# Optimization experiments

Measured on AMD Instinct MI355X. Metric: run time of the kernel, lower is better.

The kernel has to match this reference:

```python
import jax, jax.numpy as jnp
import numpy as np

N = 100000   # nodes
E = 1600000  # edges (avg degree 16)
N_IN, N_HID, N_OUT = 64, 64, 16


def setup_inputs() -> dict:
    key = jax.random.key(0)
    k1, k2, k3, k4 = jax.random.split(key, 4)
    x = jax.random.normal(k1, (N, N_IN), dtype=jnp.float32)
    edge_index = jax.random.randint(k2, (2, E), 0, N, dtype=jnp.int64)
    # Glorot-style init like PyG GCNConv linear weights
    W1 = jax.random.normal(k3, (N_IN, N_HID), dtype=jnp.float32) * (1.0 / np.sqrt(N_IN))
    b1 = jnp.zeros((N_HID,), dtype=jnp.float32)
    W2 = jax.random.normal(k4, (N_HID, N_OUT), dtype=jnp.float32) * (1.0 / np.sqrt(N_HID))
    b2 = jnp.zeros((N_OUT,), dtype=jnp.float32)
    return {"x": x, "edge_index": edge_index, "W1": W1, "b1": b1, "W2": W2, "b2": b2}


def reference(x, edge_index, W1, b1, W2, b2):
    n = x.shape[0]
    # GCNConv default: add self-loops with weight 1, symmetric normalization
    loop = jnp.arange(n, dtype=edge_index.dtype)
    src = jnp.concatenate([edge_index[0], loop])  # [E+N]
    dst = jnp.concatenate([edge_index[1], loop])  # [E+N]
    w = jnp.ones(src.shape[0], dtype=x.dtype)
    deg = jax.ops.segment_sum(w, dst, num_segments=n)           # in-degree incl. self-loop
    dinv = jnp.where(deg > 0, jax.lax.rsqrt(deg), 0.0)
    norm = dinv[src] * w * dinv[dst]                            # [E+N] edge coefficients

    def gcn_conv(h, Wm, bm):
        h = h @ Wm                                              # [N, d_out] linear first (PyG order)
        msg = h[src] * norm[:, None]                            # gather + scale
        return jax.ops.segment_sum(msg, dst, num_segments=n) + bm  # scatter-add + bias

    h = jax.nn.relu(gcn_conv(x, W1, b1))
    # dropout is identity at inference (training=False)
    return jax.nn.log_softmax(gcn_conv(h, W2, b2), axis=1)
```

## Files before the change

### kernel.cpp

```cpp
#include <hip/hip_runtime.h>

constexpr int FIN = 64;
constexpr int FH  = 64;
constexpr int FO  = 16;


constexpr int BSH      = 7;
constexpr int BW       = 1 << BSH;
constexpr int NBUCK    = 1024;
constexpr int EPB      = 4096;

constexpr int XSTR     = 68;

__device__ inline unsigned short f2bf(float f) {
    unsigned u = __float_as_uint(f);
    return (unsigned short)((u + 0x7FFFu + ((u >> 16) & 1u)) >> 16);
}
__device__ inline float bf2f(unsigned short h) {
    return __uint_as_float((unsigned)h << 16);
}
__device__ inline float4 bf4_to_f4(ushort4 u) {
    float4 f;
    f.x = bf2f(u.x); f.y = bf2f(u.y); f.z = bf2f(u.z); f.w = bf2f(u.w);
    return f;
}

__launch_bounds__(256)
__global__ void hist_kernel(const int* __restrict__ ei, int E,
                            unsigned short* __restrict__ gchist) {
    __shared__ int lh[NBUCK];
    int t = threadIdx.x;
    for (int i = t; i < NBUCK; i += 256) lh[i] = 0;
    __syncthreads();
    int base = blockIdx.x * EPB;
    int lim  = min(E, base + EPB);
    for (int e0 = base + t; e0 < lim; e0 += 2048) {
        int dd[8];
        #pragma unroll
        for (int q = 0; q < 8; ++q) {
            int e = e0 + q * 256;
            dd[q] = (e < lim) ? ei[E + e] : -1;
        }
        #pragma unroll
        for (int q = 0; q < 8; ++q)
            if (dd[q] >= 0) atomicAdd(&lh[dd[q] >> BSH], 1);
    }
    __syncthreads();
    unsigned short* gh = gchist + (size_t)blockIdx.x * NBUCK;
    for (int b = t; b < NBUCK; b += 256)
        gh[b] = (unsigned short)lh[b];
}

__launch_bounds__(1024)
__global__ void bucket_scan_kernel(const unsigned short* __restrict__ gchist,
                                   int* __restrict__ bbase, int* __restrict__ gbase,
                                   int NCH, int* __restrict__ offs, int N, int E) {
    __shared__ int s[NBUCK];
    int t = threadIdx.x;
    int v = 0;
    #pragma unroll 8
    for (int c = 0; c < NCH; ++c)
        v += (int)gchist[(size_t)c * NBUCK + t];
    s[t] = v;
    __syncthreads();
    for (int d = 1; d < NBUCK; d <<= 1) {
        int u = (t >= d) ? s[t - d] : 0;
        __syncthreads();
        s[t] += u;
        __syncthreads();
    }
    int ex = s[t] - v;
    bbase[t] = ex;
    if (t == NBUCK - 1) {
        bbase[NBUCK] = s[t];
        offs[N] = E;
    }
    int run = ex;
    #pragma unroll 8
    for (int c = 0; c < NCH; ++c) {
        gbase[(size_t)c * NBUCK + t] = run;
        run += (int)gchist[(size_t)c * NBUCK + t];
    }
}

__device__ inline void binning_body(const int* __restrict__ ei, int E, int chunk,
                                    const int* __restrict__ gbase,
                                    unsigned* __restrict__ ebuf, int* lh) {
    int t = threadIdx.x;
    const int* gb = gbase + (size_t)chunk * NBUCK;
    for (int i = t; i < NBUCK; i += 256) lh[i] = gb[i];
    __syncthreads();
    int base = chunk * EPB;
    int lim  = min(E, base + EPB);
    for (int e0 = base + t; e0 < lim; e0 += 2048) {
        int dd[8], ss[8];
        #pragma unroll
        for (int q = 0; q < 8; ++q) {
            int e = e0 + q * 256;
            if (e < lim) { dd[q] = ei[E + e]; ss[q] = ei[e]; } else dd[q] = -1;
        }
        #pragma unroll
        for (int q = 0; q < 8; ++q) {
            if (dd[q] >= 0) {
                int pos = atomicAdd(&lh[dd[q] >> BSH], 1);
                ebuf[pos] = (unsigned)ss[q] | ((unsigned)(dd[q] & (BW - 1)) << 17);
            }
        }
    }
}

__launch_bounds__(256)
__global__ void binning_kernel(const int* __restrict__ ei, int E,
                               const int* __restrict__ gbase, unsigned* __restrict__ ebuf) {
    __shared__ int lh[NBUCK];
    binning_body(ei, E, blockIdx.x, gbase, ebuf, lh);
}

__launch_bounds__(256, 4)
__global__ void gemm1_binning_kernel(const float* __restrict__ x, const float* __restrict__ W1,
                                     unsigned short* __restrict__ hsb,
                                     const int* __restrict__ ei, int E,
                                     const int* __restrict__ gbase, unsigned* __restrict__ ebuf,
                                     int N, int NBIN) {
    __shared__ float smem[FIN * FH + 64 * XSTR];
    int tid = threadIdx.x;
    if ((int)blockIdx.x < NBIN) {
        binning_body(ei, E, (int)blockIdx.x, gbase, ebuf, (int*)smem);
        return;
    }
    float* Ws = smem;
    float* Xs = smem + FIN * FH;
    int rowBase = ((int)blockIdx.x - NBIN) * 64;
    {
        const float4* W14 = (const float4*)W1;
        float4* Ws4 = (float4*)Ws;
        #pragma unroll
        for (int i = tid; i < 1024; i += 256) Ws4[i] = W14[i];
        const float4* x4 = (const float4*)x;
        #pragma unroll
        for (int i = tid; i < 1024; i += 256) {
            int row = i >> 4, kq = i & 15;
            int gr = min(rowBase + row, N - 1);
            *(float4*)&Xs[row * XSTR + kq * 4] = x4[(size_t)gr * 16 + kq];
        }
    }
    __syncthreads();
    int cg = tid & 15;
    int rg = tid >> 4;
    int r0 = rowBase + rg * 4;
    float4 acc0 = {0,0,0,0}, acc1 = {0,0,0,0}, acc2 = {0,0,0,0}, acc3 = {0,0,0,0};
    #pragma unroll 2
    for (int kc = 0; kc < 16; ++kc) {
        float4 xa0 = *(const float4*)&Xs[(rg * 4 + 0) * XSTR + kc * 4];
        float4 xa1 = *(const float4*)&Xs[(rg * 4 + 1) * XSTR + kc * 4];
        float4 xa2 = *(const float4*)&Xs[(rg * 4 + 2) * XSTR + kc * 4];
        float4 xa3 = *(const float4*)&Xs[(rg * 4 + 3) * XSTR + kc * 4];
        const float* xa0f = (const float*)&xa0;
        const float* xa1f = (const float*)&xa1;
        const float* xa2f = (const float*)&xa2;
        const float* xa3f = (const float*)&xa3;
        #pragma unroll
        for (int j = 0; j < 4; ++j) {
            float4 wv = *(const float4*)&Ws[(kc * 4 + j) * FH + cg * 4];
            float v0 = xa0f[j], v1 = xa1f[j], v2 = xa2f[j], v3 = xa3f[j];
            acc0.x = fmaf(v0, wv.x, acc0.x); acc0.y = fmaf(v0, wv.y, acc0.y);
            acc0.z = fmaf(v0, wv.z, acc0.z); acc0.w = fmaf(v0, wv.w, acc0.w);
            acc1.x = fmaf(v1, wv.x, acc1.x); acc1.y = fmaf(v1, wv.y, acc1.y);
            acc1.z = fmaf(v1, wv.z, acc1.z); acc1.w = fmaf(v1, wv.w, acc1.w);
            acc2.x = fmaf(v2, wv.x, acc2.x); acc2.y = fmaf(v2, wv.y, acc2.y);
            acc2.z = fmaf(v2, wv.z, acc2.z); acc2.w = fmaf(v2, wv.w, acc2.w);
            acc3.x = fmaf(v3, wv.x, acc3.x); acc3.y = fmaf(v3, wv.y, acc3.y);
            acc3.z = fmaf(v3, wv.z, acc3.z); acc3.w = fmaf(v3, wv.w, acc3.w);
        }
    }
    ushort4* hsb4 = (ushort4*)hsb;
    if (r0 + 0 < N) hsb4[(size_t)(r0 + 0) * 16 + cg] =
        make_ushort4(f2bf(acc0.x), f2bf(acc0.y), f2bf(acc0.z), f2bf(acc0.w));
    if (r0 + 1 < N) hsb4[(size_t)(r0 + 1) * 16 + cg] =
        make_ushort4(f2bf(acc1.x), f2bf(acc1.y), f2bf(acc1.z), f2bf(acc1.w));
    if (r0 + 2 < N) hsb4[(size_t)(r0 + 2) * 16 + cg] =
        make_ushort4(f2bf(acc2.x), f2bf(acc2.y), f2bf(acc2.z), f2bf(acc2.w));
    if (r0 + 3 < N) hsb4[(size_t)(r0 + 3) * 16 + cg] =
        make_ushort4(f2bf(acc3.x), f2bf(acc3.y), f2bf(acc3.z), f2bf(acc3.w));
}

__launch_bounds__(256)
__global__ void bucket_csr_kernel(const unsigned* __restrict__ ebuf,
                                  const int* __restrict__ bbase,
                                  int* __restrict__ csr, int* __restrict__ offs,
                                  float* __restrict__ dinv, int N) {
    __shared__ int cnt[BW], sc[BW], cur[BW];
    int t = threadIdx.x;
    int b = blockIdx.x;
    if (t < BW) cnt[t] = 0;
    __syncthreads();
    int beg = bbase[b], end = bbase[b + 1];
    for (int i0 = beg + t; i0 < end; i0 += 2048) {
        unsigned ww[8];
        #pragma unroll
        for (int q = 0; q < 8; ++q) {
            int i = i0 + q * 256;
            ww[q] = (i < end) ? ebuf[i] : 0xFFFFFFFFu;
        }
        #pragma unroll
        for (int q = 0; q < 8; ++q)
            if (ww[q] != 0xFFFFFFFFu) atomicAdd(&cnt[ww[q] >> 17], 1);
    }
    __syncthreads();
    if (t < BW) sc[t] = cnt[t];
    __syncthreads();
    for (int d = 1; d < BW; d <<= 1) {
        int u = (t < BW && t >= d) ? sc[t - d] : 0;
        __syncthreads();
        if (t < BW) sc[t] += u;
        __syncthreads();
    }
    int nodeBase = b << BSH;
    if (t < BW) {
        int node = nodeBase + t;
        int ex = beg + sc[t] - cnt[t];
        cur[t] = ex;
        if (node < N) {
            offs[node] = ex;
            dinv[node] = rsqrtf((float)(cnt[t] + 1));
        }
    }
    __syncthreads();
    for (int i0 = beg + t; i0 < end; i0 += 2048) {
        unsigned ww[8];
        #pragma unroll
        for (int q = 0; q < 8; ++q) {
            int i = i0 + q * 256;
            ww[q] = (i < end) ? ebuf[i] : 0xFFFFFFFFu;
        }
        #pragma unroll
        for (int q = 0; q < 8; ++q) {
            if (ww[q] != 0xFFFFFFFFu) {
                int pos = atomicAdd(&cur[ww[q] >> 17], 1);
                csr[pos] = (int)(ww[q] & 0x1FFFF);
            }
        }
    }
}

__launch_bounds__(256)
__global__ void agg1_gemm2_kernel(const unsigned short* __restrict__ hsb,
                                  const int* __restrict__ csr,
                                  const int* __restrict__ offs, const float* __restrict__ dinv,
                                  const float* __restrict__ b1, const float* __restrict__ W2,
                                  unsigned short* __restrict__ hs2b, int N) {
    __shared__ float W2s[FH * FO];
    __shared__ float h1s[16][68];
    const ushort4* hs4 = (const ushort4*)hsb;
    int tid = threadIdx.x;
    for (int i = tid; i < FH * FO; i += 256) W2s[i] = W2[i];
    int g = tid >> 4, l = tid & 15;
    int n = blockIdx.x * 16 + g;
    if (n < N) {
        float di_n = dinv[n];
        float4 self = bf4_to_f4(hs4[(size_t)n * 16 + l]);
        float4 acc;
        acc.x = self.x * di_n; acc.y = self.y * di_n;
        acc.z = self.z * di_n; acc.w = self.w * di_n;
        int j = offs[n], end = offs[n + 1];
        for (; j + 7 < end; j += 8) {
            int s0 = csr[j],     s1 = csr[j + 1], s2 = csr[j + 2], s3 = csr[j + 3];
            int s4 = csr[j + 4], s5 = csr[j + 5], s6 = csr[j + 6], s7 = csr[j + 7];
            float d0 = dinv[s0], d1 = dinv[s1], d2 = dinv[s2], d3 = dinv[s3];
            float d4 = dinv[s4], d5 = dinv[s5], d6 = dinv[s6], d7 = dinv[s7];
            float4 a0 = bf4_to_f4(hs4[(size_t)s0 * 16 + l]);
            float4 a1 = bf4_to_f4(hs4[(size_t)s1 * 16 + l]);
            float4 a2 = bf4_to_f4(hs4[(size_t)s2 * 16 + l]);
            float4 a3 = bf4_to_f4(hs4[(size_t)s3 * 16 + l]);
            float4 a4 = bf4_to_f4(hs4[(size_t)s4 * 16 + l]);
            float4 a5 = bf4_to_f4(hs4[(size_t)s5 * 16 + l]);
            float4 a6 = bf4_to_f4(hs4[(size_t)s6 * 16 + l]);
            float4 a7 = bf4_to_f4(hs4[(size_t)s7 * 16 + l]);
            acc.x += (fmaf(a0.x, d0, a1.x * d1) + fmaf(a2.x, d2, a3.x * d3))
                   + (fmaf(a4.x, d4, a5.x * d5) + fmaf(a6.x, d6, a7.x * d7));
            acc.y += (fmaf(a0.y, d0, a1.y * d1) + fmaf(a2.y, d2, a3.y * d3))
                   + (fmaf(a4.y, d4, a5.y * d5) + fmaf(a6.y, d6, a7.y * d7));
            acc.z += (fmaf(a0.z, d0, a1.z * d1) + fmaf(a2.z, d2, a3.z * d3))
                   + (fmaf(a4.z, d4, a5.z * d5) + fmaf(a6.z, d6, a7.z * d7));
            acc.w += (fmaf(a0.w, d0, a1.w * d1) + fmaf(a2.w, d2, a3.w * d3))
                   + (fmaf(a4.w, d4, a5.w * d5) + fmaf(a6.w, d6, a7.w * d7));
        }
        for (; j + 1 < end; j += 2) {
            int s0 = csr[j], s1 = csr[j + 1];
            float d0 = dinv[s0], d1 = dinv[s1];
            float4 a0 = bf4_to_f4(hs4[(size_t)s0 * 16 + l]);
            float4 a1 = bf4_to_f4(hs4[(size_t)s1 * 16 + l]);
            acc.x += fmaf(a0.x, d0, a1.x * d1);
            acc.y += fmaf(a0.y, d0, a1.y * d1);
            acc.z += fmaf(a0.z, d0, a1.z * d1);
            acc.w += fmaf(a0.w, d0, a1.w * d1);
        }
        if (j < end) {
            int s0 = csr[j];
            float d0 = dinv[s0];
            float4 a0 = bf4_to_f4(hs4[(size_t)s0 * 16 + l]);
            acc.x = fmaf(a0.x, d0, acc.x); acc.y = fmaf(a0.y, d0, acc.y);
            acc.z = fmaf(a0.z, d0, acc.z); acc.w = fmaf(a0.w, d0, acc.w);
        }
        float4 bb = ((const float4*)b1)[l];
        float4 h;
        h.x = fmaxf(fmaf(di_n, acc.x, bb.x), 0.f);
        h.y = fmaxf(fmaf(di_n, acc.y, bb.y), 0.f);
        h.z = fmaxf(fmaf(di_n, acc.z, bb.z), 0.f);
        h.w = fmaxf(fmaf(di_n, acc.w, bb.w), 0.f);
        *((float4*)&h1s[g][l * 4]) = h;
    }
    __syncthreads();
    int r = tid >> 4, o = tid & 15;
    int n2 = blockIdx.x * 16 + r;
    if (n2 < N) {
        float acc = 0.f;
        #pragma unroll
        for (int jj = 0; jj < FH; ++jj)
            acc = fmaf(h1s[r][jj], W2s[jj * FO + o], acc);
        hs2b[(size_t)n2 * FO + o] = f2bf(acc * dinv[n2]);
    }
}

__launch_bounds__(256)
__global__ void agg2_softmax_kernel(const unsigned short* __restrict__ hs2b,
                                    const int* __restrict__ csr,
                                    const int* __restrict__ offs, const float* __restrict__ dinv,
                                    const float* __restrict__ b2, float* __restrict__ out, int N) {
    int tid = threadIdx.x;
    int g = tid >> 4, o = tid & 15;
    int n = blockIdx.x * 16 + g;
    float v = 0.f;
    if (n < N) {
        float acc = bf2f(hs2b[(size_t)n * 16 + o]);
        int j = offs[n], end = offs[n + 1];
        for (; j + 7 < end; j += 8) {
            int s0 = csr[j],     s1 = csr[j + 1], s2 = csr[j + 2], s3 = csr[j + 3];
            int s4 = csr[j + 4], s5 = csr[j + 5], s6 = csr[j + 6], s7 = csr[j + 7];
            float t0 = bf2f(hs2b[(size_t)s0 * 16 + o]) + bf2f(hs2b[(size_t)s1 * 16 + o]);
            float t1 = bf2f(hs2b[(size_t)s2 * 16 + o]) + bf2f(hs2b[(size_t)s3 * 16 + o]);
            float t2 = bf2f(hs2b[(size_t)s4 * 16 + o]) + bf2f(hs2b[(size_t)s5 * 16 + o]);
            float t3 = bf2f(hs2b[(size_t)s6 * 16 + o]) + bf2f(hs2b[(size_t)s7 * 16 + o]);
            acc += (t0 + t1) + (t2 + t3);
        }
        for (; j < end; ++j) acc += bf2f(hs2b[(size_t)csr[j] * 16 + o]);
        v = fmaf(dinv[n], acc, b2[o]);
    }
    float m = v;
    #pragma unroll
    for (int s = 8; s >= 1; s >>= 1) m = fmaxf(m, __shfl_xor(m, s, 64));
    float ex = __expf(v - m);
    float sum = ex;
    #pragma unroll
    for (int s = 8; s >= 1; s >>= 1) sum += __shfl_xor(sum, s, 64);
    if (n < N) out[(size_t)n * FO + o] = v - m - __logf(sum);
}

extern "C" void kernel_launch(void* const* d_in, const int* in_sizes, int n_in,
                              void* d_out, int out_size, void* d_ws, size_t ws_size,
                              hipStream_t stream) {
    const float* x  = (const float*)d_in[0];
    const int*   ei = (const int*)d_in[1];
    const float* W1 = (const float*)d_in[2];
    const float* b1 = (const float*)d_in[3];
    const float* W2 = (const float*)d_in[4];
    const float* b2 = (const float*)d_in[5];
    float* out = (float*)d_out;

    const int N = in_sizes[0] / FIN;
    const int E = in_sizes[1] / 2;
    const int NCH  = (E + EPB - 1) / EPB;
    const int NB4  = (N + BW - 1) / BW;
    const int G1T  = (N + 63) / 64;
    const int GA   = (N + 15) / 16;

    char* ws = (char*)d_ws;
    size_t off = 0;
    auto alloc = [&](size_t bytes) -> void* {
        off = (off + 255) & ~(size_t)255;
        void* p = ws + off;
        off += bytes;
        return p;
    };
    float*          dinv   = (float*)alloc((size_t)N * 4);
    unsigned short* hsb    = (unsigned short*)alloc((size_t)N * FH * 2);
    unsigned short* hs2b   = (unsigned short*)alloc((size_t)N * FO * 2);
    int*            offs   = (int*)alloc((size_t)(N + 1) * 4);
    int*            bbase  = (int*)alloc((NBUCK + 1) * 4);
    unsigned short* gchist = (unsigned short*)alloc((size_t)NCH * NBUCK * 2);
    int*            gbase  = (int*)alloc((size_t)NCH * NBUCK * 4);
    unsigned* ebuf;
    int*      csr;
    bool ws_fits = (ws_size >= off + 512 + (size_t)E * 8);
    if (ws_fits) {
        ebuf = (unsigned*)alloc((size_t)E * 4);
        csr  = (int*)     alloc((size_t)E * 4);
    } else {
        ebuf = (unsigned*)x;
        csr  = (int*)x + E;
    }

    hist_kernel<<<NCH, 256, 0, stream>>>(ei, E, gchist);
    bucket_scan_kernel<<<1, NBUCK, 0, stream>>>(gchist, bbase, gbase, NCH,
                                                offs, N, E);
    if (ws_fits) {
        gemm1_binning_kernel<<<NCH + G1T, 256, 0, stream>>>(x, W1, hsb, ei, E,
                                                            gbase, ebuf, N, NCH);
    } else {
        gemm1_binning_kernel<<<G1T, 256, 0, stream>>>(x, W1, hsb, ei, E,
                                                      gbase, ebuf, N, 0);
        binning_kernel<<<NCH, 256, 0, stream>>>(ei, E, gbase, ebuf);
    }
    bucket_csr_kernel<<<NB4, 256, 0, stream>>>(ebuf, bbase, csr, offs, dinv, N);
    agg1_gemm2_kernel<<<GA, 256, 0, stream>>>(hsb, csr, offs, dinv, b1, W2, hs2b, N);
    agg2_softmax_kernel<<<GA, 256, 0, stream>>>(hs2b, csr, offs, dinv, b2, out, N);
}
```

Before: 229.9 us.

## Parallelize bucket scan with a hierarchical group-sum and chunk-base pass

The single-block bucket scan used to loop serially over all ~391 chunk histograms twice. It is now split into three stages: a multi-block group-sum over 32 chunk groups, a single-block scan over the 32 group partials, and a multi-block pass that writes the per-chunk bases. This spreads the serial histogram read and write work across many CUs. The cost is two extra kernel launches and some small extra workspace.

Measured after the change: 198.1 us. -13.8%, faster.

```diff
diff --git a/kernel.cpp b/kernel.cpp
--- a/kernel.cpp
+++ b/kernel.cpp
@@ -9,6 +9,7 @@
 constexpr int BW       = 1 << BSH;
 constexpr int NBUCK    = 1024;
 constexpr int EPB      = 4096;
+constexpr int NGRP     = 32;
 
 constexpr int XSTR     = 68;
 
@@ -51,16 +52,30 @@
         gh[b] = (unsigned short)lh[b];
 }
 
+__launch_bounds__(256)
+__global__ void group_sum_kernel(const unsigned short* __restrict__ gchist,
+                                 int* __restrict__ psum, int NCH, int CPG) {
+    int g  = blockIdx.x >> 2;
+    int br = ((blockIdx.x & 3) << 8) + threadIdx.x;
+    int c0 = g * CPG, c1 = min(NCH, c0 + CPG);
+    int s = 0;
+    #pragma unroll 4
+    for (int c = c0; c < c1; ++c)
+        s += (int)gchist[(size_t)c * NBUCK + br];
+    psum[(size_t)g * NBUCK + br] = s;
+}
+
 __launch_bounds__(1024)
-__global__ void bucket_scan_kernel(const unsigned short* __restrict__ gchist,
-                                   int* __restrict__ bbase, int* __restrict__ gbase,
-                                   int NCH, int* __restrict__ offs, int N, int E) {
+__global__ void bucket_scan_kernel(const int* __restrict__ psum,
+                                   int* __restrict__ bbase,
+                                   int* __restrict__ gbase_grp,
+                                   int* __restrict__ offs, int N, int E) {
     __shared__ int s[NBUCK];
     int t = threadIdx.x;
     int v = 0;
-    #pragma unroll 8
-    for (int c = 0; c < NCH; ++c)
-        v += (int)gchist[(size_t)c * NBUCK + t];
+    #pragma unroll
+    for (int g = 0; g < NGRP; ++g)
+        v += psum[(size_t)g * NBUCK + t];
     s[t] = v;
     __syncthreads();
     for (int d = 1; d < NBUCK; d <<= 1) {
@@ -76,10 +91,25 @@
         offs[N] = E;
     }
     int run = ex;
-    #pragma unroll 8
-    for (int c = 0; c < NCH; ++c) {
-        gbase[(size_t)c * NBUCK + t] = run;
-        run += (int)gchist[(size_t)c * NBUCK + t];
+    #pragma unroll
+    for (int g = 0; g < NGRP; ++g) {
+        gbase_grp[(size_t)g * NBUCK + t] = run;
+        run += psum[(size_t)g * NBUCK + t];
+    }
+}
+
+__launch_bounds__(256)
+__global__ void chunk_base_kernel(const unsigned short* __restrict__ gchist,
+                                  const int* __restrict__ gbase_grp,
+                                  int* __restrict__ gbase, int NCH, int CPG) {
+    int g  = blockIdx.x >> 2;
+    int br = ((blockIdx.x & 3) << 8) + threadIdx.x;
+    int c0 = g * CPG, c1 = min(NCH, c0 + CPG);
+    int run = gbase_grp[(size_t)g * NBUCK + br];
+    #pragma unroll 4
+    for (int c = c0; c < c1; ++c) {
+        gbase[(size_t)c * NBUCK + br] = run;
+        run += (int)gchist[(size_t)c * NBUCK + br];
     }
 }
 
@@ -370,6 +400,7 @@
     const int N = in_sizes[0] / FIN;
     const int E = in_sizes[1] / 2;
     const int NCH  = (E + EPB - 1) / EPB;
+    const int CPG  = (NCH + NGRP - 1) / NGRP;
     const int NB4  = (N + BW - 1) / BW;
     const int G1T  = (N + 63) / 64;
     const int GA   = (N + 15) / 16;
@@ -382,13 +413,15 @@
         off += bytes;
         return p;
     };
-    float*          dinv   = (float*)alloc((size_t)N * 4);
-    unsigned short* hsb    = (unsigned short*)alloc((size_t)N * FH * 2);
-    unsigned short* hs2b   = (unsigned short*)alloc((size_t)N * FO * 2);
-    int*            offs   = (int*)alloc((size_t)(N + 1) * 4);
-    int*            bbase  = (int*)alloc((NBUCK + 1) * 4);
-    unsigned short* gchist = (unsigned short*)alloc((size_t)NCH * NBUCK * 2);
-    int*            gbase  = (int*)alloc((size_t)NCH * NBUCK * 4);
+    float*          dinv      = (float*)alloc((size_t)N * 4);
+    unsigned short* hsb       = (unsigned short*)alloc((size_t)N * FH * 2);
+    unsigned short* hs2b      = (unsigned short*)alloc((size_t)N * FO * 2);
+    int*            offs      = (int*)alloc((size_t)(N + 1) * 4);
+    int*            bbase     = (int*)alloc((NBUCK + 1) * 4);
+    unsigned short* gchist    = (unsigned short*)alloc((size_t)NCH * NBUCK * 2);
+    int*            gbase     = (int*)alloc((size_t)NCH * NBUCK * 4);
+    int*            psum      = (int*)alloc((size_t)NGRP * NBUCK * 4);
+    int*            gbase_grp = (int*)alloc((size_t)NGRP * NBUCK * 4);
     unsigned* ebuf;
     int*      csr;
     bool ws_fits = (ws_size >= off + 512 + (size_t)E * 8);
@@ -401,8 +434,10 @@
     }
 
     hist_kernel<<<NCH, 256, 0, stream>>>(ei, E, gchist);
-    bucket_scan_kernel<<<1, NBUCK, 0, stream>>>(gchist, bbase, gbase, NCH,
-                                                offs, N, E);
+    group_sum_kernel<<<NGRP * (NBUCK / 256), 256, 0, stream>>>(gchist, psum, NCH, CPG);
+    bucket_scan_kernel<<<1, NBUCK, 0, stream>>>(psum, bbase, gbase_grp, offs, N, E);
+    chunk_base_kernel<<<NGRP * (NBUCK / 256), 256, 0, stream>>>(gchist, gbase_grp,
+                                                                gbase, NCH, CPG);
     if (ws_fits) {
         gemm1_binning_kernel<<<NCH + G1T, 256, 0, stream>>>(x, W1, hsb, ei, E,
                                                             gbase, ebuf, N, NCH);
```
